# Optimization experiments

Measured on AMD Instinct MI355X. Metric: run time of the kernel, lower is better.

The kernel has to match this reference:

```python
import jax, jax.numpy as jnp
import numpy as np

H = 16  # num_heads

def setup_inputs() -> dict:
    key = jax.random.key(0)
    ks = jax.random.split(key, 5)
    B, L, D = 2, 2048, 1024
    x = jax.random.normal(ks[0], (B, L, D), dtype=jnp.float32)
    # causal mask: masked_fill where mask == 0
    attn_mask = jnp.tril(jnp.ones((L, L), dtype=jnp.int32))
    scale = 1.0 / np.sqrt(D)
    Wq = jax.random.normal(ks[1], (D, D), dtype=jnp.float32) * scale
    Wk = jax.random.normal(ks[2], (D, D), dtype=jnp.float32) * scale
    Wv = jax.random.normal(ks[3], (D, D), dtype=jnp.float32) * scale
    Wo = jax.random.normal(ks[4], (D, D), dtype=jnp.float32) * scale
    return {"x": x, "attn_mask": attn_mask, "Wq": Wq, "Wk": Wk, "Wv": Wv, "Wo": Wo}

def reference(x, attn_mask, Wq, Wk, Wv, Wo):
    B, L, D = x.shape
    dh = D // H
    # nn.Linear with no bias: y = x @ W^T
    q = (x @ Wq.T).reshape(B, L, H, dh)
    k = (x @ Wk.T).reshape(B, L, H, dh)
    v = (x @ Wv.T).reshape(B, L, H, dh)
    # scores: [B, H, L, L]
    scores = jnp.einsum('blhd,bmhd->bhlm', q, k) / jnp.sqrt(jnp.array(dh, x.dtype))
    scores = jnp.where(attn_mask == 0, -jnp.inf, scores)
    attn = jax.nn.softmax(scores, axis=-1)
    out = jnp.einsum('bhlm,bmhd->blhd', attn, v).reshape(B, L, D)
    return out @ Wo.T
```

## Files before the change

### kernel.cpp

```cpp
#include <hip/hip_runtime.h>
#include <math.h>

#define L_SEQ  2048
#define D_MODEL 1024
#define N_HEAD 16
#define D_HEAD 64
#define B_SIZE 2

typedef __attribute__((ext_vector_type(8))) short bf16x8;
typedef __attribute__((ext_vector_type(4))) float f32x4;
typedef unsigned short u16;
typedef unsigned int u32;

__device__ __forceinline__ f32x4 mfma16(bf16x8 a, bf16x8 b, f32x4 c) {
    return __builtin_amdgcn_mfma_f32_16x16x32_bf16(a, b, c, 0, 0, 0);
}

__device__ __forceinline__ u16 f2bf(float x) {
    u32 u = __builtin_bit_cast(u32, x);
    u32 r = (u + 0x7FFFu + ((u >> 16) & 1u)) >> 16;
    return (u16)r;
}
__device__ __forceinline__ float bf2f(u16 h) {
    u32 u = ((u32)h) << 16;
    return __builtin_bit_cast(float, u);
}

__device__ __forceinline__ void gl2lds16(const void* g, void* l) {
    __builtin_amdgcn_global_load_lds(
        (__attribute__((address_space(1))) void*)(g),
        (__attribute__((address_space(3))) void*)(l), 16, 0, 0);
}

__global__ __launch_bounds__(256) void split_hl(const float* __restrict__ in,
                                                u16* __restrict__ out) {
    const int idx = blockIdx.x * 256 + threadIdx.x;
    const int c4 = idx << 2;
    const int r = c4 >> 10, c = c4 & 1023;
    float4 v = *(const float4*)(in + c4);
    u16 h0 = f2bf(v.x), h1 = f2bf(v.y), h2 = f2bf(v.z), h3 = f2bf(v.w);
    ushort4 hi = make_ushort4(h0, h1, h2, h3);
    ushort4 lo = make_ushort4(f2bf(v.x - bf2f(h0)), f2bf(v.y - bf2f(h1)),
                              f2bf(v.z - bf2f(h2)), f2bf(v.w - bf2f(h3)));
    *(ushort4*)(out + (size_t)r * 2048 + c) = hi;
    *(ushort4*)(out + (size_t)r * 2048 + 1024 + c) = lo;
}

__global__ __launch_bounds__(256) void split_w4(
    const float* __restrict__ w0, const float* __restrict__ w1,
    const float* __restrict__ w2, const float* __restrict__ w3,
    u16* __restrict__ outbase) {
    const float* in = (blockIdx.y == 0) ? w0 : (blockIdx.y == 1) ? w1
                      : (blockIdx.y == 2) ? w2 : w3;
    u16* out = outbase + (size_t)blockIdx.y * 2097152;
    const int idx = blockIdx.x * 256 + threadIdx.x;
    const int c4 = idx << 2;
    const int r = c4 >> 10, c = c4 & 1023;
    float4 v = *(const float4*)(in + c4);
    u16 h0 = f2bf(v.x), h1 = f2bf(v.y), h2 = f2bf(v.z), h3 = f2bf(v.w);
    ushort4 hi = make_ushort4(h0, h1, h2, h3);
    ushort4 lo = make_ushort4(f2bf(v.x - bf2f(h0)), f2bf(v.y - bf2f(h1)),
                              f2bf(v.z - bf2f(h2)), f2bf(v.w - bf2f(h3)));
    *(ushort4*)(out + (size_t)r * 2048 + c) = hi;
    *(ushort4*)(out + (size_t)r * 2048 + 1024 + c) = lo;
}

template <int MODE>
__global__ __launch_bounds__(256) void gemm_ks(
    const u16* __restrict__ A2, const u16* __restrict__ Wbase,
    float* __restrict__ Cout,
    u16* __restrict__ Qh, u16* __restrict__ Ql,
    u16* __restrict__ Kh, u16* __restrict__ Kl,
    u16* __restrict__ Vh, u16* __restrict__ Vl) {
    __shared__ __align__(16) u16 As[128 * 32];
    __shared__ __align__(16) u16 Ws[128 * 32];
    const int t = threadIdx.x, l = t & 63, wid = t >> 6;
    const int m0 = blockIdx.y << 7, n0 = blockIdx.x << 7;
    const int z = (MODE == 1) ? blockIdx.z : 0;
    const u16* W2 = Wbase + (size_t)z * (1024 * 2048);

    f32x4 acc[4][4];
#pragma unroll
    for (int i = 0; i < 4; ++i)
#pragma unroll
        for (int j = 0; j < 4; ++j) acc[i][j] = (f32x4){0.f, 0.f, 0.f, 0.f};

    int orow[2], ocs[2];
#pragma unroll
    for (int p = 0; p < 2; ++p) {
        int o = wid * 1024 + l * 16 + p * 4096;
        orow[p] = o >> 6;
        ocs[p] = ((o >> 4) & 3) ^ ((o >> 6) & 3);
    }
    const int wr = (wid >> 1) << 6, wc = (wid & 1) << 6;

    for (int k0 = 0; k0 < 3072; k0 += 32) {
        const int rg3 = k0 >> 10, kb = k0 & 1023;
        const int ka = (rg3 == 1 ? 1024 : 0) + kb;
        const int kw = (rg3 == 0 ? 1024 : 0) + kb;
        __syncthreads();
#pragma unroll
        for (int p = 0; p < 2; ++p) {
            gl2lds16(A2 + (size_t)(m0 + orow[p]) * 2048 + ka + ocs[p] * 8,
                     (u16*)As + (wid * 512 + p * 2048));
            gl2lds16(W2 + (size_t)(n0 + orow[p]) * 2048 + kw + ocs[p] * 8,
                     (u16*)Ws + (wid * 512 + p * 2048));
        }
        __syncthreads();
        bf16x8 af[4], bfr[4];
#pragma unroll
        for (int f = 0; f < 4; ++f) {
            int row = wr + (f << 4) + (l & 15);
            int ch = (l >> 4) ^ (row & 3);
            af[f] = *(const bf16x8*)&As[(row << 5) + (ch << 3)];
            int rown = wc + (f << 4) + (l & 15);
            int chn = (l >> 4) ^ (rown & 3);
            bfr[f] = *(const bf16x8*)&Ws[(rown << 5) + (chn << 3)];
        }
#pragma unroll
        for (int fm = 0; fm < 4; ++fm)
#pragma unroll
            for (int fn = 0; fn < 4; ++fn)
                acc[fm][fn] = mfma16(af[fm], bfr[fn], acc[fm][fn]);
    }

#pragma unroll
    for (int fm = 0; fm < 4; ++fm)
#pragma unroll
        for (int fn = 0; fn < 4; ++fn)
#pragma unroll
            for (int rg = 0; rg < 4; ++rg) {
                int gm = m0 + wr + (fm << 4) + ((l >> 4) << 2) + rg;
                int gn = n0 + wc + (fn << 4) + (l & 15);
                float v = acc[fm][fn][rg];
                if (MODE == 0) {
                    Cout[(size_t)gm * 1024 + gn] = v;
                } else {
                    if (z == 0) v *= 0.125f;
                    int b = gm >> 11, lq = gm & 2047, h = gn >> 6, d = gn & 63;
                    size_t oi = (((size_t)(b * 16 + h)) * 2048 + lq) * 64 + d;
                    u16 hi = f2bf(v);
                    u16 lo = f2bf(v - bf2f(hi));
                    u16 *ph, *pl;
                    if (z == 0)      { ph = Qh; pl = Ql; }
                    else if (z == 1) { ph = Kh; pl = Kl; }
                    else             { ph = Vh; pl = Vl; }
                    ph[oi] = hi;
                    pl[oi] = lo;
                }
            }
}

__global__ __launch_bounds__(128) void vtrans(const u16* __restrict__ Vh,
                                              const u16* __restrict__ Vl,
                                              u16* __restrict__ Vth,
                                              u16* __restrict__ Vtl) {
    const int t = threadIdx.x;
    const int kt = blockIdx.x, h = blockIdx.y, b = blockIdx.z;
    const size_t base = ((size_t)(b * 16 + h)) * 131072;
    const int kv0 = kt << 6;
    const u16* src = (t < 64) ? Vh : Vl;
    u16* dst = (t < 64) ? Vth : Vtl;
    const int st = t & 63;
    const int r0 = (st >> 3) << 3;
    const int c0 = (st & 7) << 3;
    ushort4 inv[8][2];
#pragma unroll
    for (int j = 0; j < 8; ++j) {
        const u16* p = src + base + (size_t)(kv0 + r0 + j) * 64 + c0;
        inv[j][0] = *(const ushort4*)p;
        inv[j][1] = *(const ushort4*)(p + 4);
    }
#pragma unroll
    for (int i = 0; i < 8; ++i) {
        u16 o[8];
#pragma unroll
        for (int j = 0; j < 8; ++j) {
            ushort4 vv = inv[j][i >> 2];
            const int ii = i & 3;
            o[j] = (ii == 0) ? vv.x : (ii == 1) ? vv.y : (ii == 2) ? vv.z : vv.w;
        }
        u16* q = dst + base + (size_t)(c0 + i) * 2048 + kv0 + r0;
        *(ushort4*)q = make_ushort4(o[0], o[1], o[2], o[3]);
        *(ushort4*)(q + 4) = make_ushort4(o[4], o[5], o[6], o[7]);
    }
}

struct QTileState {
    bf16x8 qhf[2], qlf[2];
    f32x4 oacc[4];
    float mrow[4], lrow[4];
};

__device__ __forceinline__ void qstate_init(
    QTileState& st, const u16* Qh, const u16* Ql, size_t hb, int q0, int w, int l) {
    const int rowq = q0 + (w << 4) + (l & 15);
#pragma unroll
    for (int kc = 0; kc < 2; ++kc) {
        const size_t off = hb + (size_t)rowq * 64 + (((kc << 2) + (l >> 4)) << 3);
        st.qhf[kc] = *(const bf16x8*)(Qh + off);
        st.qlf[kc] = *(const bf16x8*)(Ql + off);
    }
#pragma unroll
    for (int i = 0; i < 4; ++i) {
        st.oacc[i] = (f32x4){0.f, 0.f, 0.f, 0.f};
        st.mrow[i] = -INFINITY;
        st.lrow[i] = 0.f;
    }
}

__device__ __forceinline__ void fa_compute(
    QTileState& st, const u16* bKh, const u16* bKl,
    const u16* bVh, const u16* bVl, int kv0, int q0, int w, int l, u16* Pw) {
    if (kv0 > q0 + (w << 4) + 15) return;

    f32x4 sacc[4];
#pragma unroll
    for (int nf = 0; nf < 4; ++nf) sacc[nf] = (f32x4){0.f, 0.f, 0.f, 0.f};
#pragma unroll
    for (int kc = 0; kc < 2; ++kc) {
        bf16x8 kh_[4], kl_[4];
#pragma unroll
        for (int nf = 0; nf < 4; ++nf) {
            const int row = (nf << 4) + (l & 15);
            const int ch = ((kc << 2) + (l >> 4)) ^ (row & 7);
            kh_[nf] = *(const bf16x8*)&bKh[(row << 6) + (ch << 3)];
            kl_[nf] = *(const bf16x8*)&bKl[(row << 6) + (ch << 3)];
        }
#pragma unroll
        for (int nf = 0; nf < 4; ++nf) {
            sacc[nf] = mfma16(st.qhf[kc], kl_[nf], sacc[nf]);
            sacc[nf] = mfma16(st.qlf[kc], kh_[nf], sacc[nf]);
            sacc[nf] = mfma16(st.qhf[kc], kh_[nf], sacc[nf]);
        }
    }

    const bool domask = (kv0 + 63) > (q0 + (w << 4));
    float pm[4] = {-INFINITY, -INFINITY, -INFINITY, -INFINITY};
    float sv[4][4];
#pragma unroll
    for (int nf = 0; nf < 4; ++nf)
#pragma unroll
        for (int rg = 0; rg < 4; ++rg) {
            float x = sacc[nf][rg];
            if (domask) {
                const int colg = kv0 + (nf << 4) + (l & 15);
                const int rowg = q0 + (w << 4) + ((l >> 4) << 2) + rg;
                if (colg > rowg) x = -INFINITY;
            }
            sv[nf][rg] = x;
            pm[rg] = fmaxf(pm[rg], x);
        }
#pragma unroll
    for (int rg = 0; rg < 4; ++rg) {
        float v = pm[rg];
        v = fmaxf(v, __shfl_xor(v, 1));
        v = fmaxf(v, __shfl_xor(v, 2));
        v = fmaxf(v, __shfl_xor(v, 4));
        v = fmaxf(v, __shfl_xor(v, 8));
        pm[rg] = v;
    }
    float al[4];
#pragma unroll
    for (int rg = 0; rg < 4; ++rg) {
        const float mn = fmaxf(st.mrow[rg], pm[rg]);
        al[rg] = __expf(st.mrow[rg] - mn);
        st.mrow[rg] = mn;
    }
    float ps[4] = {0.f, 0.f, 0.f, 0.f};
    u16 pb[4][4];
#pragma unroll
    for (int nf = 0; nf < 4; ++nf)
#pragma unroll
        for (int rg = 0; rg < 4; ++rg) {
            const float p = __expf(sv[nf][rg] - st.mrow[rg]);
            ps[rg] += p;
            pb[nf][rg] = f2bf(p);
        }
#pragma unroll
    for (int rg = 0; rg < 4; ++rg) {
        float v = ps[rg];
        v += __shfl_xor(v, 1);
        v += __shfl_xor(v, 2);
        v += __shfl_xor(v, 4);
        v += __shfl_xor(v, 8);
        st.lrow[rg] = st.lrow[rg] * al[rg] + v;
    }
#pragma unroll
    for (int nf = 0; nf < 4; ++nf)
#pragma unroll
        for (int rg = 0; rg < 4; ++rg) st.oacc[nf][rg] *= al[rg];

#pragma unroll
    for (int nf = 0; nf < 4; ++nf)
#pragma unroll
        for (int rg = 0; rg < 4; ++rg) {
            const int r = ((l >> 4) << 2) + rg;
            const int c = (nf << 4) + (l & 15);
            const int ch = (c >> 3) ^ (r & 7);
            Pw[(r << 6) + (ch << 3) + (c & 7)] = pb[nf][rg];
        }
#pragma unroll
    for (int kc = 0; kc < 2; ++kc) {
        const int r = l & 15;
        const int chp = ((kc << 2) + (l >> 4)) ^ (r & 7);
        const bf16x8 pa = *(const bf16x8*)&Pw[(r << 6) + (chp << 3)];
        bf16x8 vh_[4], vl_[4];
#pragma unroll
        for (int nf = 0; nf < 4; ++nf) {
            const int row = (nf << 4) + (l & 15);
            const int cv = ((kc << 2) + (l >> 4)) ^ (row & 7);
            vh_[nf] = *(const bf16x8*)&bVh[(row << 6) + (cv << 3)];
            vl_[nf] = *(const bf16x8*)&bVl[(row << 6) + (cv << 3)];
        }
#pragma unroll
        for (int nf = 0; nf < 4; ++nf) {
            st.oacc[nf] = mfma16(pa, vh_[nf], st.oacc[nf]);
            st.oacc[nf] = mfma16(pa, vl_[nf], st.oacc[nf]);
        }
    }
}

__device__ __forceinline__ void fa_epilogue(
    QTileState& st, u16* A2, int g, int q0, int w, int l) {
    const int b = g >> 4, h = g & 15;
    float inv[4];
#pragma unroll
    for (int rg = 0; rg < 4; ++rg) inv[rg] = 1.0f / st.lrow[rg];
#pragma unroll
    for (int nf = 0; nf < 4; ++nf)
#pragma unroll
        for (int rg = 0; rg < 4; ++rg) {
            const int rowq = q0 + (w << 4) + ((l >> 4) << 2) + rg;
            const int m = (b << 11) + rowq;
            const int d = (nf << 4) + (l & 15);
            const float v = st.oacc[nf][rg] * inv[rg];
            const u16 hi = f2bf(v);
            const u16 lo = f2bf(v - bf2f(hi));
            const size_t rb = (size_t)m * 2048;
            A2[rb + h * 64 + d] = hi;
            A2[rb + 1024 + h * 64 + d] = lo;
        }
}

__global__ __launch_bounds__(512) void flash_mfma(
    const u16* __restrict__ Qh, const u16* __restrict__ Ql,
    const u16* __restrict__ Kh, const u16* __restrict__ Kl,
    const u16* __restrict__ Vth, const u16* __restrict__ Vtl,
    u16* __restrict__ A2) {
    extern __shared__ __align__(16) u16 smem[];
    u16* const KhsA = smem;
    u16* const KlsA = smem + 4096;
    u16* const VhsA = smem + 8192;
    u16* const VlsA = smem + 12288;
    u16* const KhsB = smem + 16384;
    u16* const KlsB = smem + 20480;
    u16* const VhsB = smem + 24576;
    u16* const VlsB = smem + 28672;
    u16* const Ps   = smem + 32768;

    const int t = threadIdx.x, l = t & 63, w = t >> 6;
    const int id = blockIdx.x;
    const int nid = ((id & 7) << 5) + (id >> 3);
    const int g = nid >> 3;
    const int p = nid & 7;
    const int q0A = p << 7;
    const int q0B = (15 - p) << 7;
    const size_t hb = (size_t)g * 131072;

    QTileState stA, stB;
    qstate_init(stA, Qh, Ql, hb, q0A, w, l);
    qstate_init(stB, Qh, Ql, hb, q0B, w, l);

    const int row_s = t >> 3;
    const int cs_s = (t & 7) ^ (row_s & 7);

    auto stage = [&](u16* dKh, u16* dKl, u16* dVh, u16* dVl, int kt_) {
        const int kv0s = kt_ << 6;
        const size_t koff = hb + (size_t)(kv0s + row_s) * 64 + cs_s * 8;
        gl2lds16(Kh + koff, dKh + t * 8);
        gl2lds16(Kl + koff, dKl + t * 8);
        const size_t voff = hb + (size_t)row_s * 2048 + kv0s + cs_s * 8;
        gl2lds16(Vth + voff, dVh + t * 8);
        gl2lds16(Vtl + voff, dVl + t * 8);
    };

    u16* const Pw = Ps + (w << 10);
    const int ntA = (p << 1) + 2;
    const int ntB = 32 - (p << 1);

    stage(KhsA, KlsA, VhsA, VlsA, 0);
    __syncthreads();
    for (int kt = 0; kt < ntB; kt += 2) {
        stage(KhsB, KlsB, VhsB, VlsB, kt + 1);
        fa_compute(stB, KhsA, KlsA, VhsA, VlsA, kt << 6, q0B, w, l, Pw);
        if (kt < ntA)
            fa_compute(stA, KhsA, KlsA, VhsA, VlsA, kt << 6, q0A, w, l, Pw);
        __syncthreads();
        if (kt + 2 < ntB) stage(KhsA, KlsA, VhsA, VlsA, kt + 2);
        fa_compute(stB, KhsB, KlsB, VhsB, VlsB, (kt + 1) << 6, q0B, w, l, Pw);
        if (kt + 1 < ntA)
            fa_compute(stA, KhsB, KlsB, VhsB, VlsB, (kt + 1) << 6, q0A, w, l, Pw);
        __syncthreads();
    }

    fa_epilogue(stA, A2, g, q0A, w, l);
    fa_epilogue(stB, A2, g, q0B, w, l);
}

__global__ __launch_bounds__(256) void gemm_bt_f32(
    const float* __restrict__ A, const float* __restrict__ W,
    float* __restrict__ C, int M, int N, int K) {
    __shared__ float As[16][68];
    __shared__ float Bs[16][68];
    const int t = threadIdx.x;
    const int tx = t & 15, ty = t >> 4;
    const int m0 = blockIdx.y << 6, n0 = blockIdx.x << 6;
    const int lr = t >> 2, lc = (t & 3) << 2;
    const float* Ag = A + (size_t)(m0 + lr) * K + lc;
    const float* Wg = W + (size_t)(n0 + lr) * K + lc;
    float acc[4][4];
#pragma unroll
    for (int i = 0; i < 4; ++i)
#pragma unroll
        for (int j = 0; j < 4; ++j) acc[i][j] = 0.f;
    for (int k0 = 0; k0 < K; k0 += 16) {
        const float4 av = *(const float4*)(Ag + k0);
        const float4 wv = *(const float4*)(Wg + k0);
        __syncthreads();
        As[lc + 0][lr] = av.x; As[lc + 1][lr] = av.y;
        As[lc + 2][lr] = av.z; As[lc + 3][lr] = av.w;
        Bs[lc + 0][lr] = wv.x; Bs[lc + 1][lr] = wv.y;
        Bs[lc + 2][lr] = wv.z; Bs[lc + 3][lr] = wv.w;
        __syncthreads();
#pragma unroll
        for (int kk = 0; kk < 16; ++kk) {
            const float4 a = *(const float4*)&As[kk][ty << 2];
            const float4 b = *(const float4*)&Bs[kk][tx << 2];
            acc[0][0] += a.x * b.x; acc[0][1] += a.x * b.y; acc[0][2] += a.x * b.z; acc[0][3] += a.x * b.w;
            acc[1][0] += a.y * b.x; acc[1][1] += a.y * b.y; acc[1][2] += a.y * b.z; acc[1][3] += a.y * b.w;
            acc[2][0] += a.z * b.x; acc[2][1] += a.z * b.y; acc[2][2] += a.z * b.z; acc[2][3] += a.z * b.w;
            acc[3][0] += a.w * b.x; acc[3][1] += a.w * b.y; acc[3][2] += a.w * b.z; acc[3][3] += a.w * b.w;
        }
    }
#pragma unroll
    for (int i = 0; i < 4; ++i) {
        float4 o;
        o.x = acc[i][0]; o.y = acc[i][1]; o.z = acc[i][2]; o.w = acc[i][3];
        *(float4*)&C[(size_t)(m0 + (ty << 2) + i) * N + n0 + (tx << 2)] = o;
    }
}

#define SW(row, seg) ((((seg) ^ (((row) + ((row) >> 4)) & 15)) << 2))

__global__ __launch_bounds__(256) void flash_f32(
    const float* __restrict__ Q, const float* __restrict__ K,
    const float* __restrict__ V, float* __restrict__ O) {
    __shared__ float Qs[64 * 64];
    __shared__ float KPs[64 * 64];
    __shared__ float Vs[64 * 64];
    const int t = threadIdx.x;
    const int tx = t & 15, ty = t >> 4;
    const int qt = blockIdx.x, h = blockIdx.y, b = blockIdx.z;
    const int q0 = qt << 6;
    const size_t hbase = (size_t)b * L_SEQ * D_MODEL + (size_t)h * D_HEAD;
#pragma unroll
    for (int i = 0; i < 4; ++i) {
        const int idx = t + (i << 8);
        const int rr = idx >> 4, seg = idx & 15;
        const float4 qv = *(const float4*)&Q[hbase + (size_t)(q0 + rr) * D_MODEL + (seg << 2)];
        *(float4*)&Qs[rr * 64 + SW(rr, seg)] = qv;
    }
    float m[4], lr_[4], oacc[4][4];
#pragma unroll
    for (int i = 0; i < 4; ++i) {
        m[i] = -INFINITY; lr_[i] = 0.f;
#pragma unroll
        for (int j = 0; j < 4; ++j) oacc[i][j] = 0.f;
    }
    const int ntile = qt + 1;
    for (int kt = 0; kt < ntile; ++kt) {
        const int kv0 = kt << 6;
        __syncthreads();
#pragma unroll
        for (int i = 0; i < 4; ++i) {
            const int idx = t + (i << 8);
            const int rr = idx >> 4, seg = idx & 15;
            const float4 kv = *(const float4*)&K[hbase + (size_t)(kv0 + rr) * D_MODEL + (seg << 2)];
            const float4 vv = *(const float4*)&V[hbase + (size_t)(kv0 + rr) * D_MODEL + (seg << 2)];
            *(float4*)&KPs[rr * 64 + SW(rr, seg)] = kv;
            *(float4*)&Vs[rr * 64 + SW(rr, seg)] = vv;
        }
        __syncthreads();
        float s[4][4];
#pragma unroll
        for (int i = 0; i < 4; ++i)
#pragma unroll
            for (int j = 0; j < 4; ++j) s[i][j] = 0.f;
#pragma unroll
        for (int seg = 0; seg < 16; ++seg) {
            float4 qv[4], kv[4];
#pragma unroll
            for (int i = 0; i < 4; ++i) {
                const int R = (ty << 2) + i;
                qv[i] = *(const float4*)&Qs[R * 64 + SW(R, seg)];
            }
#pragma unroll
            for (int j = 0; j < 4; ++j) {
                const int Cc = (tx << 2) + j;
                kv[j] = *(const float4*)&KPs[Cc * 64 + SW(Cc, seg)];
            }
#pragma unroll
            for (int i = 0; i < 4; ++i)
#pragma unroll
                for (int j = 0; j < 4; ++j)
                    s[i][j] += qv[i].x * kv[j].x + qv[i].y * kv[j].y +
                               qv[i].z * kv[j].z + qv[i].w * kv[j].w;
        }
        const bool diag = (kt == qt);
        float tm[4];
#pragma unroll
        for (int i = 0; i < 4; ++i) {
            tm[i] = -INFINITY;
#pragma unroll
            for (int j = 0; j < 4; ++j) {
                float sval = s[i][j] * 0.125f;
                if (diag) {
                    const int Cg = kv0 + (tx << 2) + j;
                    const int Rg = q0 + (ty << 2) + i;
                    if (Cg > Rg) sval = -INFINITY;
                }
                s[i][j] = sval;
                tm[i] = fmaxf(tm[i], sval);
            }
            tm[i] = fmaxf(tm[i], __shfl_xor(tm[i], 1));
            tm[i] = fmaxf(tm[i], __shfl_xor(tm[i], 2));
            tm[i] = fmaxf(tm[i], __shfl_xor(tm[i], 4));
            tm[i] = fmaxf(tm[i], __shfl_xor(tm[i], 8));
        }
        float p[4][4];
#pragma unroll
        for (int i = 0; i < 4; ++i) {
            const float mn = fmaxf(m[i], tm[i]);
            const float alpha = __expf(m[i] - mn);
            m[i] = mn;
            float psum = 0.f;
#pragma unroll
            for (int j = 0; j < 4; ++j) {
                p[i][j] = __expf(s[i][j] - mn);
                psum += p[i][j];
            }
            psum += __shfl_xor(psum, 1);
            psum += __shfl_xor(psum, 2);
            psum += __shfl_xor(psum, 4);
            psum += __shfl_xor(psum, 8);
            lr_[i] = lr_[i] * alpha + psum;
#pragma unroll
            for (int j = 0; j < 4; ++j) oacc[i][j] *= alpha;
        }
        __syncthreads();
#pragma unroll
        for (int i = 0; i < 4; ++i) {
            const int R = (ty << 2) + i;
            float4 pv;
            pv.x = p[i][0]; pv.y = p[i][1]; pv.z = p[i][2]; pv.w = p[i][3];
            *(float4*)&KPs[R * 64 + SW(R, tx)] = pv;
        }
        __syncthreads();
#pragma unroll
        for (int cs = 0; cs < 16; ++cs) {
            float pc[4][4];
            float4 vr[4];
#pragma unroll
            for (int i = 0; i < 4; ++i) {
                const int R = (ty << 2) + i;
                const float4 pr = *(const float4*)&KPs[R * 64 + SW(R, cs)];
                pc[i][0] = pr.x; pc[i][1] = pr.y; pc[i][2] = pr.z; pc[i][3] = pr.w;
            }
#pragma unroll
            for (int cc = 0; cc < 4; ++cc) {
                const int Cr = (cs << 2) + cc;
                vr[cc] = *(const float4*)&Vs[Cr * 64 + SW(Cr, tx)];
            }
#pragma unroll
            for (int i = 0; i < 4; ++i)
#pragma unroll
                for (int cc = 0; cc < 4; ++cc) {
                    oacc[i][0] += pc[i][cc] * vr[cc].x;
                    oacc[i][1] += pc[i][cc] * vr[cc].y;
                    oacc[i][2] += pc[i][cc] * vr[cc].z;
                    oacc[i][3] += pc[i][cc] * vr[cc].w;
                }
        }
    }
#pragma unroll
    for (int i = 0; i < 4; ++i) {
        const int R = (ty << 2) + i;
        const float invl = 1.0f / lr_[i];
        float4 o;
        o.x = oacc[i][0] * invl; o.y = oacc[i][1] * invl;
        o.z = oacc[i][2] * invl; o.w = oacc[i][3] * invl;
        *(float4*)&O[hbase + (size_t)(q0 + R) * D_MODEL + (tx << 2)] = o;
    }
}

extern "C" void kernel_launch(void* const* d_in, const int* in_sizes, int n_in,
                              void* d_out, int out_size, void* d_ws, size_t ws_size,
                              hipStream_t stream) {
    const float* x  = (const float*)d_in[0];
    const float* Wq = (const float*)d_in[2];
    const float* Wk = (const float*)d_in[3];
    const float* Wv = (const float*)d_in[4];
    const float* Wo = (const float*)d_in[5];
    float* out = (float*)d_out;

    if (ws_size >= 83886080ull) {
        char* ws = (char*)d_ws;
        u16* x2  = (u16*)(ws);
        u16* Wq2 = (u16*)(ws + 16777216);
        u16* Wo2 = (u16*)(ws + 29360128);
        u16* Qh  = (u16*)(ws + 33554432);
        u16* Ql  = (u16*)(ws + 41943040);
        u16* Kh  = (u16*)(ws + 50331648);
        u16* Kl  = (u16*)(ws + 58720256);
        u16* Vth = (u16*)(ws + 67108864);
        u16* Vtl = (u16*)(ws + 75497472);
        u16* Vh  = (u16*)d_out;
        u16* Vl  = (u16*)d_out + 4194304;

        hipFuncSetAttribute((const void*)flash_mfma,
                            hipFuncAttributeMaxDynamicSharedMemorySize, 81920);

        split_hl<<<4096, 256, 0, stream>>>(x, x2);
        split_w4<<<dim3(1024, 4), 256, 0, stream>>>(Wq, Wk, Wv, Wo, Wq2);
        gemm_ks<1><<<dim3(8, 32, 3), 256, 0, stream>>>(x2, Wq2, nullptr,
                                                       Qh, Ql, Kh, Kl, Vh, Vl);
        vtrans<<<dim3(32, 16, 2), 128, 0, stream>>>(Vh, Vl, Vth, Vtl);
        flash_mfma<<<256, 512, 81920, stream>>>(Qh, Ql, Kh, Kl, Vth, Vtl, x2);
        gemm_ks<0><<<dim3(8, 32, 1), 256, 0, stream>>>(x2, Wo2, out,
                                                       nullptr, nullptr, nullptr,
                                                       nullptr, nullptr, nullptr);
    } else {
        const int M = B_SIZE * L_SEQ, N = D_MODEL, Kd = D_MODEL;
        float* Qw = (float*)d_ws;
        float* Kw = Qw + (size_t)M * D_MODEL;
        float* Vw = Kw + (size_t)M * D_MODEL;
        float* Aw = Vw + (size_t)M * D_MODEL;
        dim3 gg(N / 64, M / 64);
        gemm_bt_f32<<<gg, 256, 0, stream>>>(x, Wq, Qw, M, N, Kd);
        gemm_bt_f32<<<gg, 256, 0, stream>>>(x, Wk, Kw, M, N, Kd);
        gemm_bt_f32<<<gg, 256, 0, stream>>>(x, Wv, Vw, M, N, Kd);
        flash_f32<<<dim3(L_SEQ / 64, N_HEAD, B_SIZE), 256, 0, stream>>>(Qw, Kw, Vw, Aw);
        gemm_bt_f32<<<gg, 256, 0, stream>>>(Aw, Wo, out, M, N, Kd);
    }
}
```

Baseline: 260.5 us.

## Split flash attention blocks into 64-row Q tiles and raise MFMA priority

The flash attention kernel now launches 512 blocks of 256 threads instead of 256 blocks of 512, each block handling a pair of 64-row query tiles balanced across the causal triangle. KV staging runs in two passes per thread, the loop handles odd tile counts, and LDS per block shrinks. s_setprio is raised around the MFMA sequences so waves issuing matrix ops are favoured over waves doing loads. The aim is more blocks per CU and better load balance and latency hiding, at the cost of each block reusing every staged K/V tile for fewer query rows.

```diff
diff --git a/kernel.cpp b/kernel.cpp
--- a/kernel.cpp
+++ b/kernel.cpp
@@ -227,12 +227,14 @@
             kh_[nf] = *(const bf16x8*)&bKh[(row << 6) + (ch << 3)];
             kl_[nf] = *(const bf16x8*)&bKl[(row << 6) + (ch << 3)];
         }
+        __builtin_amdgcn_s_setprio(1);
 #pragma unroll
         for (int nf = 0; nf < 4; ++nf) {
             sacc[nf] = mfma16(st.qhf[kc], kl_[nf], sacc[nf]);
             sacc[nf] = mfma16(st.qlf[kc], kh_[nf], sacc[nf]);
             sacc[nf] = mfma16(st.qhf[kc], kh_[nf], sacc[nf]);
         }
+        __builtin_amdgcn_s_setprio(0);
     }
 
     const bool domask = (kv0 + 63) > (q0 + (w << 4));
@@ -313,11 +315,13 @@
             vh_[nf] = *(const bf16x8*)&bVh[(row << 6) + (cv << 3)];
             vl_[nf] = *(const bf16x8*)&bVl[(row << 6) + (cv << 3)];
         }
+        __builtin_amdgcn_s_setprio(1);
 #pragma unroll
         for (int nf = 0; nf < 4; ++nf) {
             st.oacc[nf] = mfma16(pa, vh_[nf], st.oacc[nf]);
             st.oacc[nf] = mfma16(pa, vl_[nf], st.oacc[nf]);
         }
+        __builtin_amdgcn_s_setprio(0);
     }
 }
 
@@ -343,7 +347,7 @@
         }
 }
 
-__global__ __launch_bounds__(512) void flash_mfma(
+__global__ __launch_bounds__(256) void flash_mfma(
     const u16* __restrict__ Qh, const u16* __restrict__ Ql,
     const u16* __restrict__ Kh, const u16* __restrict__ Kl,
     const u16* __restrict__ Vth, const u16* __restrict__ Vtl,
@@ -361,47 +365,56 @@
 
     const int t = threadIdx.x, l = t & 63, w = t >> 6;
     const int id = blockIdx.x;
-    const int nid = ((id & 7) << 5) + (id >> 3);
-    const int g = nid >> 3;
-    const int p = nid & 7;
-    const int q0A = p << 7;
-    const int q0B = (15 - p) << 7;
+    const int nid = ((id & 7) << 6) + (id >> 3);
+    const int g = nid >> 4;
+    const int rem = nid & 15;
+    const int p = rem >> 1;
+    const int s = rem & 1;
+    const int q0A = (p << 7) + (s << 6);
+    const int q0B = ((15 - p) << 7) + ((1 - s) << 6);
     const size_t hb = (size_t)g * 131072;
 
     QTileState stA, stB;
     qstate_init(stA, Qh, Ql, hb, q0A, w, l);
     qstate_init(stB, Qh, Ql, hb, q0B, w, l);
 
-    const int row_s = t >> 3;
-    const int cs_s = (t & 7) ^ (row_s & 7);
-
     auto stage = [&](u16* dKh, u16* dKl, u16* dVh, u16* dVl, int kt_) {
         const int kv0s = kt_ << 6;
-        const size_t koff = hb + (size_t)(kv0s + row_s) * 64 + cs_s * 8;
-        gl2lds16(Kh + koff, dKh + t * 8);
-        gl2lds16(Kl + koff, dKl + t * 8);
-        const size_t voff = hb + (size_t)row_s * 2048 + kv0s + cs_s * 8;
-        gl2lds16(Vth + voff, dVh + t * 8);
-        gl2lds16(Vtl + voff, dVl + t * 8);
+#pragma unroll
+        for (int pass = 0; pass < 2; ++pass) {
+            const int o = t + (pass << 8);
+            const int row = o >> 3;
+            const int cs = (o & 7) ^ (row & 7);
+            const int dofs = o << 3;
+            const size_t koff = hb + (size_t)(kv0s + row) * 64 + cs * 8;
+            gl2lds16(Kh + koff, dKh + dofs);
+            gl2lds16(Kl + koff, dKl + dofs);
+            const size_t voff = hb + (size_t)row * 2048 + kv0s + cs * 8;
+            gl2lds16(Vth + voff, dVh + dofs);
+            gl2lds16(Vtl + voff, dVl + dofs);
+        }
     };
 
     u16* const Pw = Ps + (w << 10);
-    const int ntA = (p << 1) + 2;
-    const int ntB = 32 - (p << 1);
+    const int ntA = (q0A >> 6) + 1;
+    const int ntB = (q0B >> 6) + 1;
 
     stage(KhsA, KlsA, VhsA, VlsA, 0);
     __syncthreads();
     for (int kt = 0; kt < ntB; kt += 2) {
-        stage(KhsB, KlsB, VhsB, VlsB, kt + 1);
+        const bool has1 = (kt + 1 < ntB);
+        if (has1) stage(KhsB, KlsB, VhsB, VlsB, kt + 1);
         fa_compute(stB, KhsA, KlsA, VhsA, VlsA, kt << 6, q0B, w, l, Pw);
         if (kt < ntA)
             fa_compute(stA, KhsA, KlsA, VhsA, VlsA, kt << 6, q0A, w, l, Pw);
         __syncthreads();
-        if (kt + 2 < ntB) stage(KhsA, KlsA, VhsA, VlsA, kt + 2);
-        fa_compute(stB, KhsB, KlsB, VhsB, VlsB, (kt + 1) << 6, q0B, w, l, Pw);
-        if (kt + 1 < ntA)
-            fa_compute(stA, KhsB, KlsB, VhsB, VlsB, (kt + 1) << 6, q0A, w, l, Pw);
-        __syncthreads();
+        if (has1) {
+            if (kt + 2 < ntB) stage(KhsA, KlsA, VhsA, VlsA, kt + 2);
+            fa_compute(stB, KhsB, KlsB, VhsB, VlsB, (kt + 1) << 6, q0B, w, l, Pw);
+            if (kt + 1 < ntA)
+                fa_compute(stA, KhsB, KlsB, VhsB, VlsB, (kt + 1) << 6, q0A, w, l, Pw);
+            __syncthreads();
+        }
     }
 
     fa_epilogue(stA, A2, g, q0A, w, l);
@@ -629,14 +642,14 @@
         u16* Vl  = (u16*)d_out + 4194304;
 
         hipFuncSetAttribute((const void*)flash_mfma,
-                            hipFuncAttributeMaxDynamicSharedMemorySize, 81920);
+                            hipFuncAttributeMaxDynamicSharedMemorySize, 73728);
 
         split_hl<<<4096, 256, 0, stream>>>(x, x2);
         split_w4<<<dim3(1024, 4), 256, 0, stream>>>(Wq, Wk, Wv, Wo, Wq2);
         gemm_ks<1><<<dim3(8, 32, 3), 256, 0, stream>>>(x2, Wq2, nullptr,
                                                        Qh, Ql, Kh, Kl, Vh, Vl);
         vtrans<<<dim3(32, 16, 2), 128, 0, stream>>>(Vh, Vl, Vth, Vtl);
-        flash_mfma<<<256, 512, 81920, stream>>>(Qh, Ql, Kh, Kl, Vth, Vtl, x2);
+        flash_mfma<<<512, 256, 73728, stream>>>(Qh, Ql, Kh, Kl, Vth, Vtl, x2);
         gemm_ks<0><<<dim3(8, 32, 1), 256, 0, stream>>>(x2, Wo2, out,
                                                        nullptr, nullptr, nullptr,
                                                        nullptr, nullptr, nullptr);
```

Result: slower. 272.7 us (+4.7%).
